# Kernel tuning notes

Hardware: AMD Instinct MI355X
Metric: run time of the kernel (lower is better)

Reference implementation:

```python
import jax, jax.numpy as jnp
import numpy as np

N_NODES, N_EDGES, H = 25000, 400000, 64
EPS = 1e-15


def _norm(x):
    return jnp.sqrt(jnp.sum(x * x, axis=-1, keepdims=True))


def _projx(x, c):
    norm = _norm(x)
    max_norm = (1.0 - 1e-5) / jnp.sqrt(c)
    scale = jnp.minimum(max_norm / jnp.maximum(norm, EPS), 1.0)
    return x * scale


def _expmap0(x, c):
    norm = _norm(x)
    sc = jnp.sqrt(c)
    return jnp.tanh(sc * norm) * x / (norm * sc + EPS)


def _logmap0(x, c):
    norm = _norm(x)
    sc = jnp.sqrt(c)
    return (1.0 / sc) * jnp.arctanh(jnp.minimum(sc * norm, 1.0 - 1e-5)) * x / (norm + EPS)


def _mobius_add(x, y, c):
    x2 = jnp.sum(x * x, axis=-1, keepdims=True)
    y2 = jnp.sum(y * y, axis=-1, keepdims=True)
    xy = jnp.sum(x * y, axis=-1, keepdims=True)
    num = (1.0 + 2.0 * c * xy + c * y2) * x + (1.0 - c * x2) * y
    denom = 1.0 + 2.0 * c * xy + c * c * x2 * y2
    return num / (denom + EPS)


def _mobius_linear(x, W, b, c):
    t = _logmap0(x, c)
    out = t @ W.T + b
    return _expmap0(out, c)


def setup_inputs() -> dict:
    key = jax.random.key(0)
    ks = jax.random.split(key, 12)
    h_V = jax.random.normal(ks[0], (N_NODES, H), dtype=jnp.float32) * 0.3
    h_E = jax.random.normal(ks[1], (N_EDGES, 3 * H), dtype=jnp.float32) * 0.3
    src = jax.random.randint(ks[2], (N_EDGES,), 0, N_NODES, dtype=jnp.int32)
    dst = jax.random.randint(ks[3], (N_EDGES,), 0, N_NODES, dtype=jnp.int32)
    log_c = jnp.zeros((), dtype=jnp.float32)  # c = 1.0

    def lin(k, out_d, in_d):
        bound = 1.0 / np.sqrt(in_d)
        kw, kb = jax.random.split(k)
        W = jax.random.uniform(kw, (out_d, in_d), jnp.float32, -bound, bound)
        b = jax.random.uniform(kb, (out_d,), jnp.float32, -bound, bound)
        return W, b

    W1_w, W1_b = lin(ks[4], H, 5 * H)
    W2_w, W2_b = lin(ks[5], H, H)
    W3_w, W3_b = lin(ks[6], H, H)
    return {"h_V": h_V, "h_E": h_E, "src": src, "dst": dst, "log_c": log_c,
            "W1_w": W1_w, "W1_b": W1_b, "W2_w": W2_w, "W2_b": W2_b,
            "W3_w": W3_w, "W3_b": W3_b}


def reference(h_V, h_E, src, dst, log_c, W1_w, W1_b, W2_w, W2_b, W3_w, W3_b):
    c = jnp.exp(log_c)
    n_nodes = h_V.shape[0]
    h_E = _projx(h_E, c)
    h_V = _projx(h_V, c)
    # edge gather -> fused mobius-linear chain  [E, 5H] -> [E, H]
    h_EV = jnp.concatenate([h_E, h_V[src], h_V[dst]], axis=-1)
    h_EV = _mobius_linear(h_EV, W1_w, W1_b, c)
    h_EV = _mobius_linear(_projx(jax.nn.relu(h_EV), c), W2_w, W2_b, c)
    h_msg = _mobius_linear(_projx(jax.nn.relu(h_EV), c), W3_w, W3_b, c)
    # hyperbolic aggregate: logmap0 -> scatter-mean over src -> expmap0
    tangent = _logmap0(h_msg, c)
    sums = jax.ops.segment_sum(tangent, src, num_segments=n_nodes)
    counts = jax.ops.segment_sum(jnp.ones((tangent.shape[0],), tangent.dtype), src,
                                 num_segments=n_nodes)
    agg_t = sums / jnp.maximum(counts, 1.0)[:, None]
    agg = _expmap0(agg_t, c)
    h_V = _mobius_add(h_V, agg, c)  # dropout disabled (eval)
    return _projx(h_V, c)
```

## Files before the change

### kernel.cpp

```cpp
#include <hip/hip_runtime.h>
#include <hip/hip_bf16.h>
#include <math.h>

#define EPSF 1e-15f

typedef __attribute__((ext_vector_type(8))) short bf16x8;
typedef __attribute__((ext_vector_type(4))) float f32x4;

__device__ __forceinline__ unsigned short f2bf(float x) {
    unsigned u = __float_as_uint(x);
    u += 0x7fffu + ((u >> 16) & 1u);
    return (unsigned short)(u >> 16);
}
__device__ __forceinline__ float bf2f(unsigned short b) {
    return __uint_as_float(((unsigned)b) << 16);
}
__device__ __forceinline__ unsigned pkbf(float lo, float hi) {
    __hip_bfloat162 h = __float22bfloat162_rn(make_float2(lo, hi));
    return *reinterpret_cast<unsigned*>(&h);
}
__device__ __forceinline__ float fast_tanh_pos(float x) {
    if (x < 0.25f) { float x2 = x * x; return x * (1.0f - x2 * (0.33333334f - 0.13333334f * x2)); }
    float e = __expf(2.0f * x);
    return 1.0f - 2.0f / (e + 1.0f);
}
__device__ __forceinline__ float fast_atanh01(float y) {
    if (y < 0.125f) { float y2 = y * y; return y * (1.0f + y2 * (0.33333334f + 0.2f * y2)); }
    return 0.5f * __logf((1.0f + y) / (1.0f - y));
}

__device__ __forceinline__ float wred(float v) {
#pragma unroll
    for (int off = 32; off; off >>= 1) v += __shfl_xor(v, off);
    return v;
}

__global__ void prep_wfrag(const float* __restrict__ W1, const float* __restrict__ W2,
                           const float* __restrict__ W3, unsigned short* __restrict__ Wf) {
    int idx = blockIdx.x * blockDim.x + threadIdx.x;
    if (idx >= 56 * 64) return;
    int fid = idx >> 6, lane = idx & 63;
    int i15 = lane & 15, grp = lane >> 4;
    unsigned short* dstp = Wf + ((size_t)fid * 64 + lane) * 8;
    if (fid < 40) {
        int ks = fid >> 2, t = fid & 3;
        int n = t * 16 + i15;
        int k0 = ks * 32 + grp * 8;
#pragma unroll
        for (int i = 0; i < 8; ++i) dstp[i] = f2bf(W1[n * 320 + k0 + i]);
    } else {
        const float* srcW = (fid < 48) ? W2 : W3;
        int b = (fid < 48) ? fid - 40 : fid - 48;
        int s2 = b >> 2, t = b & 3;
        int n = t * 16 + i15;
#pragma unroll
        for (int i = 0; i < 8; ++i) {
            int kp = 16 * (2 * s2 + (i >> 2)) + 4 * grp + (i & 3);
            dstp[i] = f2bf(srcW[n * 64 + kp]);
        }
    }
}

__global__ void __launch_bounds__(256)
node_prep(const float* __restrict__ hV, const float* __restrict__ logc,
          unsigned short* __restrict__ hVp, float* __restrict__ pj, int n_nodes) {
    int wid  = (blockIdx.x * blockDim.x + threadIdx.x) >> 6;
    int lane = threadIdx.x & 63;
    if (wid >= n_nodes) return;
    float c    = __expf(logc[0]);
    float scq  = sqrtf(c);
    float maxn = (1.0f - 1e-5f) / scq;
    float x = hV[(size_t)wid * 64 + lane];
    float p = wred(x * x);
    float sS = fminf(maxn / fmaxf(sqrtf(p), EPSF), 1.0f);
    hVp[(size_t)wid * 64 + lane] = f2bf(x * sS);
    if (lane == 0) pj[wid] = sS * sS * p;
}

__global__ void hist_kernel(const int* __restrict__ src, int* __restrict__ cnt,
                            int* __restrict__ slot, int n_edges) {
    int e = blockIdx.x * blockDim.x + threadIdx.x;
    if (e < n_edges) slot[e] = atomicAdd(&cnt[src[e]], 1);
}

__global__ void __launch_bounds__(1024)
scan_rowptr(const int* __restrict__ cnt, int* __restrict__ rowptr, int n) {
    __shared__ int wpart[16];
    int C   = (n + 1023) >> 10;
    int tid = threadIdx.x;
    int beg = tid * C;
    int end = beg + C; if (end > n) end = n;
    int s = 0;
    if (beg < n) for (int k = beg; k < end; ++k) s += cnt[k];
    int lane = tid & 63, wv = tid >> 6;
    int v = s;
#pragma unroll
    for (int off = 1; off < 64; off <<= 1) {
        int t = __shfl_up(v, off);
        if (lane >= off) v += t;
    }
    if (lane == 63) wpart[wv] = v;
    __syncthreads();
    if (tid < 64) {
        int t = (tid < 16) ? wpart[tid] : 0;
#pragma unroll
        for (int off = 1; off < 16; off <<= 1) {
            int u = __shfl_up(t, off);
            if (lane >= off) t += u;
        }
        if (tid < 16) wpart[tid] = t;
    }
    __syncthreads();
    int base = (wv ? wpart[wv - 1] : 0) + (v - s);
    if (beg < n) {
        int run = base;
        for (int k = beg; k < end; ++k) { rowptr[k] = run; run += cnt[k]; }
    }
    if (tid == 1023) rowptr[n] = wpart[15];
}

__global__ void slotfix_kernel(const int* __restrict__ src, const int* __restrict__ rowptr,
                               int* __restrict__ slot, int n_edges) {
    int e = blockIdx.x * blockDim.x + threadIdx.x;
    if (e < n_edges) slot[e] += rowptr[src[e]];
}

__device__ __forceinline__ void stage_mlp_t(float (&v)[4][4],
                                            const bf16x8* __restrict__ Wfrag, int fbase,
                                            const float* __restrict__ bvec,
                                            float scq, float maxn, int grp) {
    float n2 = 0.f, rn2 = 0.f;
    float u[4][4];
#pragma unroll
    for (int t = 0; t < 4; ++t)
#pragma unroll
        for (int r = 0; r < 4; ++r) {
            float x = v[t][r];
            n2 = fmaf(x, x, n2);
            float y = fmaxf(x, 0.f);
            u[t][r] = y;
            rn2 = fmaf(y, y, rn2);
        }
    n2  += __shfl_xor(n2, 16);  n2  += __shfl_xor(n2, 32);
    rn2 += __shfl_xor(rn2, 16); rn2 += __shfl_xor(rn2, 32);
    float n  = sqrtf(n2);
    float h  = fast_tanh_pos(scq * n) / (n * scq + EPSF);
    float rn = h * sqrtf(rn2);
    float ps = fminf(maxn / fmaxf(rn, EPSF), 1.0f);
    float pn = rn * ps;
    float gg = fast_atanh01(fminf(scq * pn, 1.0f - 1e-5f)) / (scq * (pn + EPSF));
    float f2 = h * ps * gg;

    union { bf16x8 b; unsigned w[4]; } B0, B1;
    B0.w[0] = pkbf(u[0][0], u[0][1]); B0.w[1] = pkbf(u[0][2], u[0][3]);
    B0.w[2] = pkbf(u[1][0], u[1][1]); B0.w[3] = pkbf(u[1][2], u[1][3]);
    B1.w[0] = pkbf(u[2][0], u[2][1]); B1.w[1] = pkbf(u[2][2], u[2][3]);
    B1.w[2] = pkbf(u[3][0], u[3][1]); B1.w[3] = pkbf(u[3][2], u[3][3]);

    f32x4 acc[4] = {};
#pragma unroll
    for (int t = 0; t < 4; ++t)
        acc[t] = __builtin_amdgcn_mfma_f32_16x16x32_bf16(
            Wfrag[(size_t)(fbase + t) * 64 + (grp * 16 + (threadIdx.x & 15))], B0.b, acc[t], 0, 0, 0);
#pragma unroll
    for (int t = 0; t < 4; ++t)
        acc[t] = __builtin_amdgcn_mfma_f32_16x16x32_bf16(
            Wfrag[(size_t)(fbase + 4 + t) * 64 + (grp * 16 + (threadIdx.x & 15))], B1.b, acc[t], 0, 0, 0);

#pragma unroll
    for (int t = 0; t < 4; ++t) {
        const float4 bv = *reinterpret_cast<const float4*>(&bvec[t * 16 + 4 * grp]);
        v[t][0] = fmaf(f2, acc[t][0], bv.x);
        v[t][1] = fmaf(f2, acc[t][1], bv.y);
        v[t][2] = fmaf(f2, acc[t][2], bv.z);
        v[t][3] = fmaf(f2, acc[t][3], bv.w);
    }
}

__global__ void __launch_bounds__(256)
edge_mfma(const float* __restrict__ hE, const int* __restrict__ src,
          const int* __restrict__ dst, const float* __restrict__ logc,
          const unsigned short* __restrict__ Wf, const unsigned short* __restrict__ hVp,
          const float* __restrict__ pj,
          const float* __restrict__ b1, const float* __restrict__ b2,
          const float* __restrict__ b3, const int* __restrict__ slot,
          unsigned short* __restrict__ tg, int n_edges) {
    int lane = threadIdx.x & 63;
    int w    = threadIdx.x >> 6;
    int tile = blockIdx.x * 4 + w;
    int e0 = tile * 16;
    if (e0 >= n_edges) return;

    float c    = __expf(logc[0]);
    float scq  = sqrtf(c);
    float maxn = (1.0f - 1e-5f) / scq;

    int i15 = lane & 15, grp = lane >> 4;
    int ev = e0 + i15; if (ev >= n_edges) ev = n_edges - 1;
    int s16 = src[ev], d16 = dst[ev];

    const bf16x8* Wfrag = reinterpret_cast<const bf16x8*>(Wf);

    const bf16x8* vsp = reinterpret_cast<const bf16x8*>(hVp + (size_t)s16 * 64);
    const bf16x8* vdp = reinterpret_cast<const bf16x8*>(hVp + (size_t)d16 * 64);
    bf16x8 aS0 = vsp[grp], aS1 = vsp[4 + grp];
    bf16x8 aD0 = vdp[grp], aD1 = vdp[4 + grp];
    float pjS = pj[s16], pjD = pj[d16];

    float pE = 0.f;
    bf16x8 aE[6];
    const float* eb = hE + (size_t)ev * 192;
#pragma unroll
    for (int ks = 0; ks < 6; ++ks) {
        const float4* p4 = reinterpret_cast<const float4*>(eb + ks * 32 + grp * 8);
        float4 a0 = p4[0], a1 = p4[1];
        pE += a0.x*a0.x + a0.y*a0.y + a0.z*a0.z + a0.w*a0.w
            + a1.x*a1.x + a1.y*a1.y + a1.z*a1.z + a1.w*a1.w;
        union { bf16x8 b; unsigned u[4]; } cv;
        cv.u[0] = pkbf(a0.x, a0.y);
        cv.u[1] = pkbf(a0.z, a0.w);
        cv.u[2] = pkbf(a1.x, a1.y);
        cv.u[3] = pkbf(a1.z, a1.w);
        aE[ks] = cv.b;
    }
    pE += __shfl_xor(pE, 16); pE += __shfl_xor(pE, 32);
    float sE = fminf(maxn / fmaxf(sqrtf(pE), EPSF), 1.0f);
    float nt = sqrtf(sE * sE * pE + pjS + pjD);
    float gq = fast_atanh01(fminf(scq * nt, 1.0f - 1e-5f)) / (scq * (nt + EPSF));

    f32x4 accE[4] = {}, accV[4] = {};
#pragma unroll
    for (int ks = 0; ks < 6; ++ks) {
#pragma unroll
        for (int t = 0; t < 4; ++t)
            accE[t] = __builtin_amdgcn_mfma_f32_16x16x32_bf16(
                Wfrag[(size_t)(ks * 4 + t) * 64 + lane], aE[ks], accE[t], 0, 0, 0);
    }
#pragma unroll
    for (int t = 0; t < 4; ++t)
        accV[t] = __builtin_amdgcn_mfma_f32_16x16x32_bf16(
            Wfrag[(size_t)(24 + t) * 64 + lane], aS0, accV[t], 0, 0, 0);
#pragma unroll
    for (int t = 0; t < 4; ++t)
        accV[t] = __builtin_amdgcn_mfma_f32_16x16x32_bf16(
            Wfrag[(size_t)(28 + t) * 64 + lane], aS1, accV[t], 0, 0, 0);
#pragma unroll
    for (int t = 0; t < 4; ++t)
        accV[t] = __builtin_amdgcn_mfma_f32_16x16x32_bf16(
            Wfrag[(size_t)(32 + t) * 64 + lane], aD0, accV[t], 0, 0, 0);
#pragma unroll
    for (int t = 0; t < 4; ++t)
        accV[t] = __builtin_amdgcn_mfma_f32_16x16x32_bf16(
            Wfrag[(size_t)(36 + t) * 64 + lane], aD1, accV[t], 0, 0, 0);

    float v[4][4];
#pragma unroll
    for (int t = 0; t < 4; ++t) {
        const float4 bv = *reinterpret_cast<const float4*>(&b1[t * 16 + 4 * grp]);
        v[t][0] = fmaf(gq, fmaf(sE, accE[t][0], accV[t][0]), bv.x);
        v[t][1] = fmaf(gq, fmaf(sE, accE[t][1], accV[t][1]), bv.y);
        v[t][2] = fmaf(gq, fmaf(sE, accE[t][2], accV[t][2]), bv.z);
        v[t][3] = fmaf(gq, fmaf(sE, accE[t][3], accV[t][3]), bv.w);
    }

    stage_mlp_t(v, Wfrag, 40, b2, scq, maxn, grp);
    stage_mlp_t(v, Wfrag, 48, b3, scq, maxn, grp);

    float n2 = 0.f;
#pragma unroll
    for (int t = 0; t < 4; ++t)
#pragma unroll
        for (int r = 0; r < 4; ++r) n2 = fmaf(v[t][r], v[t][r], n2);
    n2 += __shfl_xor(n2, 16); n2 += __shfl_xor(n2, 32);
    float n  = sqrtf(n2);
    float h  = fast_tanh_pos(scq * n) / (n * scq + EPSF);
    float hn = h * n;
    float g4 = fast_atanh01(fminf(scq * hn, 1.0f - 1e-5f)) / (scq * (hn + EPSF));
    float fT = g4 * h;

    if (e0 + i15 < n_edges) {
        int sl = slot[ev];
        unsigned short* orow = tg + (size_t)sl * 64;
#pragma unroll
        for (int t = 0; t < 4; ++t) {
            uint2 o;
            o.x = pkbf(fT * v[t][0], fT * v[t][1]);
            o.y = pkbf(fT * v[t][2], fT * v[t][3]);
            *reinterpret_cast<uint2*>(&orow[t * 16 + 4 * grp]) = o;
        }
    }
}

__global__ void __launch_bounds__(256)
node_gather(const float* __restrict__ hV, const float* __restrict__ logc,
            const unsigned short* __restrict__ tg, const int* __restrict__ rowptr,
            float* __restrict__ out, int n_nodes) {
    int wid  = (blockIdx.x * blockDim.x + threadIdx.x) >> 6;
    int lane = threadIdx.x & 63;
    if (wid >= n_nodes) return;

    float c    = __expf(logc[0]);
    float scq  = sqrtf(c);
    float maxn = (1.0f - 1e-5f) / scq;

    int beg = rowptr[wid], end = rowptr[wid + 1];
    int g = lane >> 4, i15 = lane & 15;
    float s0 = 0.f, s1 = 0.f, s2 = 0.f, s3 = 0.f;
    for (int i = beg + g; i < end; i += 4) {
        uint2 p = *reinterpret_cast<const uint2*>(&tg[(size_t)i * 64 + i15 * 4]);
        s0 += bf2f((unsigned short)(p.x & 0xffff));
        s1 += bf2f((unsigned short)(p.x >> 16));
        s2 += bf2f((unsigned short)(p.y & 0xffff));
        s3 += bf2f((unsigned short)(p.y >> 16));
    }
    s0 += __shfl_xor(s0, 16); s0 += __shfl_xor(s0, 32);
    s1 += __shfl_xor(s1, 16); s1 += __shfl_xor(s1, 32);
    s2 += __shfl_xor(s2, 16); s2 += __shfl_xor(s2, 32);
    s3 += __shfl_xor(s3, 16); s3 += __shfl_xor(s3, 32);
    int srcl = lane >> 2;
    float a0 = __shfl(s0, srcl), a1 = __shfl(s1, srcl);
    float a2 = __shfl(s2, srcl), a3 = __shfl(s3, srcl);
    float ssum = (lane & 2) ? ((lane & 1) ? a3 : a2) : ((lane & 1) ? a1 : a0);

    float inv = 1.f / fmaxf((float)(end - beg), 1.f);
    float at  = ssum * inv;

    float an2 = wred(at * at);
    float an  = sqrtf(an2);
    float ae  = fast_tanh_pos(scq * an) / (an * scq + EPSF);

    float xv  = hV[(size_t)wid * 64 + lane];
    float hs2 = wred(xv * xv);
    float sX  = fminf(maxn / fmaxf(sqrtf(hs2), EPSF), 1.0f);

    float x = sX * xv, y = ae * at;
    float x2 = wred(x * x);
    float y2 = wred(y * y);
    float xy = wred(x * y);

    float ca = 1.f + 2.f * c * xy + c * y2;
    float cb = 1.f - c * x2;
    float id = 1.f / (1.f + 2.f * c * xy + c * c * x2 * y2 + EPSF);

    float r   = (ca * x + cb * y) * id;
    float rn2 = wred(r * r);
    float rs  = fminf(maxn / fmaxf(sqrtf(rn2), EPSF), 1.0f);

    out[(size_t)wid * 64 + lane] = rs * r;
}

extern "C" void kernel_launch(void* const* d_in, const int* in_sizes, int n_in,
                              void* d_out, int out_size, void* d_ws, size_t ws_size,
                              hipStream_t stream) {
    const float* hV   = (const float*)d_in[0];
    const float* hE   = (const float*)d_in[1];
    const int*   src  = (const int*)d_in[2];
    const int*   dst  = (const int*)d_in[3];
    const float* logc = (const float*)d_in[4];
    const float* W1   = (const float*)d_in[5];
    const float* b1   = (const float*)d_in[6];
    const float* W2   = (const float*)d_in[7];
    const float* b2   = (const float*)d_in[8];
    const float* W3   = (const float*)d_in[9];
    const float* b3   = (const float*)d_in[10];

    int n_nodes = in_sizes[0] / 64;
    int n_edges = in_sizes[2];
    float* out = (float*)d_out;

    char* wsb = (char*)d_ws;
    unsigned short* Wf = (unsigned short*)wsb;
    size_t off = 56 * 512 * sizeof(unsigned short);
    int* cnt    = (int*)(wsb + off);   off += (size_t)n_nodes * 4;
    int* rowptr = (int*)(wsb + off);   off += (size_t)(n_nodes + 1) * 4;
    int* slot   = (int*)(wsb + off);   off += (size_t)n_edges * 4;
    float* pj   = (float*)(wsb + off); off += (size_t)n_nodes * 4;
    off = (off + 15) & ~(size_t)15;
    unsigned short* hVp = (unsigned short*)(wsb + off);
    off += (size_t)n_nodes * 64 * 2;
    off = (off + 15) & ~(size_t)15;
    unsigned short* tg = (unsigned short*)(wsb + off);

    hipMemsetAsync(cnt, 0, (size_t)n_nodes * sizeof(int), stream);

    prep_wfrag<<<(56 * 64 + 255) / 256, 256, 0, stream>>>(W1, W2, W3, Wf);
    node_prep<<<(n_nodes + 3) / 4, 256, 0, stream>>>(hV, logc, hVp, pj, n_nodes);
    hist_kernel<<<(n_edges + 255) / 256, 256, 0, stream>>>(src, cnt, slot, n_edges);
    scan_rowptr<<<1, 1024, 0, stream>>>(cnt, rowptr, n_nodes);
    slotfix_kernel<<<(n_edges + 255) / 256, 256, 0, stream>>>(src, rowptr, slot, n_edges);

    int tiles = (n_edges + 15) / 16;
    edge_mfma<<<(tiles + 3) / 4, 256, 0, stream>>>(
        hE, src, dst, logc, Wf, hVp, pj, b1, b2, b3, slot, tg, n_edges);

    node_gather<<<(n_nodes + 3) / 4, 256, 0, stream>>>(
        hV, logc, tg, rowptr, out, n_nodes);
}
```

Before: 237.4 us.

## Switch edge MLP to 32x32x16 MFMA with 32-edge tiles per wave

Replaces the 16x16x32 bf16 MFMA tiling with 32x32x16 MFMA, so each wave handles 32 edges instead of 16, and re-lays out the weight fragments to match. The edge-feature loads are now interleaved with the first-layer MFMAs instead of buffered first. Norm reductions need one shuffle instead of two. The aim is to halve the weight-fragment loads per edge and issue fewer instructions. In exchange it uses more accumulator registers (two 16-wide accumulators per matrix), which may lower occupancy, and launches half as many waves.

```diff
diff --git a/kernel.cpp b/kernel.cpp
--- a/kernel.cpp
+++ b/kernel.cpp
@@ -5,7 +5,7 @@
 #define EPSF 1e-15f
 
 typedef __attribute__((ext_vector_type(8))) short bf16x8;
-typedef __attribute__((ext_vector_type(4))) float f32x4;
+typedef __attribute__((ext_vector_type(16))) float f32x16;
 
 __device__ __forceinline__ unsigned short f2bf(float x) {
     unsigned u = __float_as_uint(x);
@@ -40,24 +40,22 @@
     int idx = blockIdx.x * blockDim.x + threadIdx.x;
     if (idx >= 56 * 64) return;
     int fid = idx >> 6, lane = idx & 63;
-    int i15 = lane & 15, grp = lane >> 4;
+    int e31 = lane & 31, hi = lane >> 5;
     unsigned short* dstp = Wf + ((size_t)fid * 64 + lane) * 8;
     if (fid < 40) {
-        int ks = fid >> 2, t = fid & 3;
-        int n = t * 16 + i15;
-        int k0 = ks * 32 + grp * 8;
+        int ks = fid >> 1, t = fid & 1;
+        int n = 32 * t + e31;
+        int k0 = 16 * ks + 8 * hi;
 #pragma unroll
         for (int i = 0; i < 8; ++i) dstp[i] = f2bf(W1[n * 320 + k0 + i]);
     } else {
         const float* srcW = (fid < 48) ? W2 : W3;
         int b = (fid < 48) ? fid - 40 : fid - 48;
-        int s2 = b >> 2, t = b & 3;
-        int n = t * 16 + i15;
-#pragma unroll
-        for (int i = 0; i < 8; ++i) {
-            int kp = 16 * (2 * s2 + (i >> 2)) + 4 * grp + (i & 3);
-            dstp[i] = f2bf(srcW[n * 64 + kp]);
-        }
+        int ks = b >> 1, t2 = b & 1;
+        int n = 32 * t2 + e31;
+        int cb = 32 * (ks >> 1) + 16 * (ks & 1) + 4 * hi;
+#pragma unroll
+        for (int i = 0; i < 8; ++i) dstp[i] = f2bf(srcW[n * 64 + cb + 8 * (i >> 2) + (i & 3)]);
     }
 }
 
@@ -125,24 +123,24 @@
     if (e < n_edges) slot[e] += rowptr[src[e]];
 }
 
-__device__ __forceinline__ void stage_mlp_t(float (&v)[4][4],
+__device__ __forceinline__ void stage_mlp32(float (&v)[2][16],
                                             const bf16x8* __restrict__ Wfrag, int fbase,
                                             const float* __restrict__ bvec,
-                                            float scq, float maxn, int grp) {
+                                            float scq, float maxn, int lane, int hi) {
     float n2 = 0.f, rn2 = 0.f;
-    float u[4][4];
-#pragma unroll
-    for (int t = 0; t < 4; ++t)
-#pragma unroll
-        for (int r = 0; r < 4; ++r) {
-            float x = v[t][r];
+    float u[2][16];
+#pragma unroll
+    for (int t = 0; t < 2; ++t)
+#pragma unroll
+        for (int j = 0; j < 16; ++j) {
+            float x = v[t][j];
             n2 = fmaf(x, x, n2);
             float y = fmaxf(x, 0.f);
-            u[t][r] = y;
+            u[t][j] = y;
             rn2 = fmaf(y, y, rn2);
         }
-    n2  += __shfl_xor(n2, 16);  n2  += __shfl_xor(n2, 32);
-    rn2 += __shfl_xor(rn2, 16); rn2 += __shfl_xor(rn2, 32);
+    n2  += __shfl_xor(n2, 32);
+    rn2 += __shfl_xor(rn2, 32);
     float n  = sqrtf(n2);
     float h  = fast_tanh_pos(scq * n) / (n * scq + EPSF);
     float rn = h * sqrtf(rn2);
@@ -151,30 +149,30 @@
     float gg = fast_atanh01(fminf(scq * pn, 1.0f - 1e-5f)) / (scq * (pn + EPSF));
     float f2 = h * ps * gg;
 
-    union { bf16x8 b; unsigned w[4]; } B0, B1;
-    B0.w[0] = pkbf(u[0][0], u[0][1]); B0.w[1] = pkbf(u[0][2], u[0][3]);
-    B0.w[2] = pkbf(u[1][0], u[1][1]); B0.w[3] = pkbf(u[1][2], u[1][3]);
-    B1.w[0] = pkbf(u[2][0], u[2][1]); B1.w[1] = pkbf(u[2][2], u[2][3]);
-    B1.w[2] = pkbf(u[3][0], u[3][1]); B1.w[3] = pkbf(u[3][2], u[3][3]);
-
-    f32x4 acc[4] = {};
-#pragma unroll
-    for (int t = 0; t < 4; ++t)
-        acc[t] = __builtin_amdgcn_mfma_f32_16x16x32_bf16(
-            Wfrag[(size_t)(fbase + t) * 64 + (grp * 16 + (threadIdx.x & 15))], B0.b, acc[t], 0, 0, 0);
-#pragma unroll
-    for (int t = 0; t < 4; ++t)
-        acc[t] = __builtin_amdgcn_mfma_f32_16x16x32_bf16(
-            Wfrag[(size_t)(fbase + 4 + t) * 64 + (grp * 16 + (threadIdx.x & 15))], B1.b, acc[t], 0, 0, 0);
-
-#pragma unroll
-    for (int t = 0; t < 4; ++t) {
-        const float4 bv = *reinterpret_cast<const float4*>(&bvec[t * 16 + 4 * grp]);
-        v[t][0] = fmaf(f2, acc[t][0], bv.x);
-        v[t][1] = fmaf(f2, acc[t][1], bv.y);
-        v[t][2] = fmaf(f2, acc[t][2], bv.z);
-        v[t][3] = fmaf(f2, acc[t][3], bv.w);
-    }
+    f32x16 acc[2] = {};
+#pragma unroll
+    for (int ks = 0; ks < 4; ++ks) {
+        int t = ks >> 1, jb = 8 * (ks & 1);
+        union { bf16x8 b; unsigned w[4]; } B;
+        B.w[0] = pkbf(u[t][jb + 0], u[t][jb + 1]);
+        B.w[1] = pkbf(u[t][jb + 2], u[t][jb + 3]);
+        B.w[2] = pkbf(u[t][jb + 4], u[t][jb + 5]);
+        B.w[3] = pkbf(u[t][jb + 6], u[t][jb + 7]);
+#pragma unroll
+        for (int t2 = 0; t2 < 2; ++t2)
+            acc[t2] = __builtin_amdgcn_mfma_f32_32x32x16_bf16(
+                Wfrag[(size_t)(fbase + ks * 2 + t2) * 64 + lane], B.b, acc[t2], 0, 0, 0);
+    }
+#pragma unroll
+    for (int t2 = 0; t2 < 2; ++t2)
+#pragma unroll
+        for (int q = 0; q < 4; ++q) {
+            const float4 bv = *reinterpret_cast<const float4*>(&bvec[32 * t2 + 8 * q + 4 * hi]);
+            v[t2][4 * q + 0] = fmaf(f2, acc[t2][4 * q + 0], bv.x);
+            v[t2][4 * q + 1] = fmaf(f2, acc[t2][4 * q + 1], bv.y);
+            v[t2][4 * q + 2] = fmaf(f2, acc[t2][4 * q + 2], bv.z);
+            v[t2][4 * q + 3] = fmaf(f2, acc[t2][4 * q + 3], bv.w);
+        }
 }
 
 __global__ void __launch_bounds__(256)
@@ -188,31 +186,32 @@
     int lane = threadIdx.x & 63;
     int w    = threadIdx.x >> 6;
     int tile = blockIdx.x * 4 + w;
-    int e0 = tile * 16;
+    int e0 = tile * 32;
     if (e0 >= n_edges) return;
 
     float c    = __expf(logc[0]);
     float scq  = sqrtf(c);
     float maxn = (1.0f - 1e-5f) / scq;
 
-    int i15 = lane & 15, grp = lane >> 4;
-    int ev = e0 + i15; if (ev >= n_edges) ev = n_edges - 1;
+    int e31 = lane & 31, hi = lane >> 5;
+    int ev = e0 + e31; if (ev >= n_edges) ev = n_edges - 1;
     int s16 = src[ev], d16 = dst[ev];
+    float pjS = pj[s16], pjD = pj[d16];
 
     const bf16x8* Wfrag = reinterpret_cast<const bf16x8*>(Wf);
 
     const bf16x8* vsp = reinterpret_cast<const bf16x8*>(hVp + (size_t)s16 * 64);
     const bf16x8* vdp = reinterpret_cast<const bf16x8*>(hVp + (size_t)d16 * 64);
-    bf16x8 aS0 = vsp[grp], aS1 = vsp[4 + grp];
-    bf16x8 aD0 = vdp[grp], aD1 = vdp[4 + grp];
-    float pjS = pj[s16], pjD = pj[d16];
-
+    bf16x8 aS[4], aD[4];
+#pragma unroll
+    for (int q = 0; q < 4; ++q) { aS[q] = vsp[2 * q + hi]; aD[q] = vdp[2 * q + hi]; }
+
+    f32x16 accE[2] = {}, accV[2] = {};
     float pE = 0.f;
-    bf16x8 aE[6];
-    const float* eb = hE + (size_t)ev * 192;
-#pragma unroll
-    for (int ks = 0; ks < 6; ++ks) {
-        const float4* p4 = reinterpret_cast<const float4*>(eb + ks * 32 + grp * 8);
+    const float* eb = hE + (size_t)ev * 192 + 8 * hi;
+#pragma unroll
+    for (int ks = 0; ks < 12; ++ks) {
+        const float4* p4 = reinterpret_cast<const float4*>(eb + 16 * ks);
         float4 a0 = p4[0], a1 = p4[1];
         pE += a0.x*a0.x + a0.y*a0.y + a0.z*a0.z + a0.w*a0.w
             + a1.x*a1.x + a1.y*a1.y + a1.z*a1.z + a1.w*a1.w;
@@ -221,73 +220,70 @@
         cv.u[1] = pkbf(a0.z, a0.w);
         cv.u[2] = pkbf(a1.x, a1.y);
         cv.u[3] = pkbf(a1.z, a1.w);
-        aE[ks] = cv.b;
-    }
-    pE += __shfl_xor(pE, 16); pE += __shfl_xor(pE, 32);
+#pragma unroll
+        for (int t = 0; t < 2; ++t)
+            accE[t] = __builtin_amdgcn_mfma_f32_32x32x16_bf16(
+                Wfrag[(size_t)(ks * 2 + t) * 64 + lane], cv.b, accE[t], 0, 0, 0);
+    }
+#pragma unroll
+    for (int q = 0; q < 4; ++q) {
+#pragma unroll
+        for (int t = 0; t < 2; ++t)
+            accV[t] = __builtin_amdgcn_mfma_f32_32x32x16_bf16(
+                Wfrag[(size_t)((12 + q) * 2 + t) * 64 + lane], aS[q], accV[t], 0, 0, 0);
+    }
+#pragma unroll
+    for (int q = 0; q < 4; ++q) {
+#pragma unroll
+        for (int t = 0; t < 2; ++t)
+            accV[t] = __builtin_amdgcn_mfma_f32_32x32x16_bf16(
+                Wfrag[(size_t)((16 + q) * 2 + t) * 64 + lane], aD[q], accV[t], 0, 0, 0);
+    }
+
+    pE += __shfl_xor(pE, 32);
     float sE = fminf(maxn / fmaxf(sqrtf(pE), EPSF), 1.0f);
     float nt = sqrtf(sE * sE * pE + pjS + pjD);
     float gq = fast_atanh01(fminf(scq * nt, 1.0f - 1e-5f)) / (scq * (nt + EPSF));
 
-    f32x4 accE[4] = {}, accV[4] = {};
-#pragma unroll
-    for (int ks = 0; ks < 6; ++ks) {
-#pragma unroll
-        for (int t = 0; t < 4; ++t)
-            accE[t] = __builtin_amdgcn_mfma_f32_16x16x32_bf16(
-                Wfrag[(size_t)(ks * 4 + t) * 64 + lane], aE[ks], accE[t], 0, 0, 0);
-    }
-#pragma unroll
-    for (int t = 0; t < 4; ++t)
-        accV[t] = __builtin_amdgcn_mfma_f32_16x16x32_bf16(
-            Wfrag[(size_t)(24 + t) * 64 + lane], aS0, accV[t], 0, 0, 0);
-#pragma unroll
-    for (int t = 0; t < 4; ++t)
-        accV[t] = __builtin_amdgcn_mfma_f32_16x16x32_bf16(
-            Wfrag[(size_t)(28 + t) * 64 + lane], aS1, accV[t], 0, 0, 0);
-#pragma unroll
-    for (int t = 0; t < 4; ++t)
-        accV[t] = __builtin_amdgcn_mfma_f32_16x16x32_bf16(
-            Wfrag[(size_t)(32 + t) * 64 + lane], aD0, accV[t], 0, 0, 0);
-#pragma unroll
-    for (int t = 0; t < 4; ++t)
-        accV[t] = __builtin_amdgcn_mfma_f32_16x16x32_bf16(
-            Wfrag[(size_t)(36 + t) * 64 + lane], aD1, accV[t], 0, 0, 0);
-
-    float v[4][4];
-#pragma unroll
-    for (int t = 0; t < 4; ++t) {
-        const float4 bv = *reinterpret_cast<const float4*>(&b1[t * 16 + 4 * grp]);
-        v[t][0] = fmaf(gq, fmaf(sE, accE[t][0], accV[t][0]), bv.x);
-        v[t][1] = fmaf(gq, fmaf(sE, accE[t][1], accV[t][1]), bv.y);
-        v[t][2] = fmaf(gq, fmaf(sE, accE[t][2], accV[t][2]), bv.z);
-        v[t][3] = fmaf(gq, fmaf(sE, accE[t][3], accV[t][3]), bv.w);
-    }
-
-    stage_mlp_t(v, Wfrag, 40, b2, scq, maxn, grp);
-    stage_mlp_t(v, Wfrag, 48, b3, scq, maxn, grp);
+    float v[2][16];
+#pragma unroll
+    for (int t = 0; t < 2; ++t)
+#pragma unroll
+        for (int q = 0; q < 4; ++q) {
+            const float4 bv = *reinterpret_cast<const float4*>(&b1[32 * t + 8 * q + 4 * hi]);
+            v[t][4*q+0] = fmaf(gq, fmaf(sE, accE[t][4*q+0], accV[t][4*q+0]), bv.x);
+            v[t][4*q+1] = fmaf(gq, fmaf(sE, accE[t][4*q+1], accV[t][4*q+1]), bv.y);
+            v[t][4*q+2] = fmaf(gq, fmaf(sE, accE[t][4*q+2], accV[t][4*q+2]), bv.z);
+            v[t][4*q+3] = fmaf(gq, fmaf(sE, accE[t][4*q+3], accV[t][4*q+3]), bv.w);
+        }
+
+    stage_mlp32(v, Wfrag, 40, b2, scq, maxn, lane, hi);
+    stage_mlp32(v, Wfrag, 48, b3, scq, maxn, lane, hi);
 
     float n2 = 0.f;
 #pragma unroll
-    for (int t = 0; t < 4; ++t)
-#pragma unroll
-        for (int r = 0; r < 4; ++r) n2 = fmaf(v[t][r], v[t][r], n2);
-    n2 += __shfl_xor(n2, 16); n2 += __shfl_xor(n2, 32);
+    for (int t = 0; t < 2; ++t)
+#pragma unroll
+        for (int j = 0; j < 16; ++j) n2 = fmaf(v[t][j], v[t][j], n2);
+    n2 += __shfl_xor(n2, 32);
     float n  = sqrtf(n2);
     float h  = fast_tanh_pos(scq * n) / (n * scq + EPSF);
     float hn = h * n;
     float g4 = fast_atanh01(fminf(scq * hn, 1.0f - 1e-5f)) / (scq * (hn + EPSF));
     float fT = g4 * h;
 
-    if (e0 + i15 < n_edges) {
+    if (e0 + e31 < n_edges) {
         int sl = slot[ev];
         unsigned short* orow = tg + (size_t)sl * 64;
 #pragma unroll
-        for (int t = 0; t < 4; ++t) {
-            uint2 o;
-            o.x = pkbf(fT * v[t][0], fT * v[t][1]);
-            o.y = pkbf(fT * v[t][2], fT * v[t][3]);
-            *reinterpret_cast<uint2*>(&orow[t * 16 + 4 * grp]) = o;
-        }
+        for (int t = 0; t < 2; ++t)
+#pragma unroll
+            for (int q = 0; q < 4; ++q) {
+                uint2 o;
+                o.x = pkbf(fT * v[t][4*q+0], fT * v[t][4*q+1]);
+                o.y = pkbf(fT * v[t][4*q+2], fT * v[t][4*q+3]);
+                *reinterpret_cast<uint2*>(&orow[32 * t + 8 * q + 4 * hi]) = o;
+            }
     }
 }
 
@@ -389,7 +385,7 @@
     scan_rowptr<<<1, 1024, 0, stream>>>(cnt, rowptr, n_nodes);
     slotfix_kernel<<<(n_edges + 255) / 256, 256, 0, stream>>>(src, rowptr, slot, n_edges);
 
-    int tiles = (n_edges + 15) / 16;
+    int tiles = (n_edges + 31) / 32;
     edge_mfma<<<(tiles + 3) / 4, 256, 0, stream>>>(
         hE, src, dst, logc, Wf, hVp, pj, b1, b2, b3, slot, tg, n_edges);
 
```

After: 242.3 us. +2.1%, slower.
